# Optimization experiments

Measured on AMD Instinct MI355X. Metric: run time of the kernel, lower is better.

Reference implementation:

```python
import jax, jax.numpy as jnp
import numpy as np

B, T, EPROJS, DUNITS, ATT_DIM, ODIM, LMAX = 16, 800, 512, 1024, 512, 5000, 96
SOS = EOS = ODIM - 1
SCALING = 2.0  # ESPnet AttAdd default softmax scaling


def setup_inputs() -> dict:
    key = jax.random.key(0)
    ks = jax.random.split(key, 16)
    w = lambda i, shape: (jax.random.normal(ks[i], shape, jnp.float32) * 0.02)
    return {
        "hs_pad": jax.random.normal(ks[0], (B, T, EPROJS), jnp.float32),
        "hlens": jnp.full((B,), T, dtype=jnp.int32),
        "ys_pad": jax.random.randint(ks[1], (B, LMAX), 0, ODIM - 2, dtype=jnp.int32),
        "embed": w(2, (ODIM, DUNITS)),
        # layer 0 LSTMCell: input = [embed ; att_context]
        "W_ih0": w(3, (4 * DUNITS, DUNITS + EPROJS)),
        "W_hh0": w(4, (4 * DUNITS, DUNITS)),
        "b_ih0": jnp.zeros((4 * DUNITS,), jnp.float32),
        "b_hh0": jnp.zeros((4 * DUNITS,), jnp.float32),
        # layer 1 LSTMCell
        "W_ih1": w(5, (4 * DUNITS, DUNITS)),
        "W_hh1": w(6, (4 * DUNITS, DUNITS)),
        "b_ih1": jnp.zeros((4 * DUNITS,), jnp.float32),
        "b_hh1": jnp.zeros((4 * DUNITS,), jnp.float32),
        # AttAdd (additive attention)
        "W_enc": w(7, (ATT_DIM, EPROJS)),
        "b_enc": jnp.zeros((ATT_DIM,), jnp.float32),
        "W_dec": w(8, (ATT_DIM, DUNITS)),
        "gvec": w(9, (ATT_DIM,)),
        # output projection (context_residual=False -> dunits -> odim)
        "W_out": w(10, (ODIM, DUNITS)),
        "b_out": jnp.zeros((ODIM,), jnp.float32),
    }


def _lstm_cell(x, h, c, W_ih, W_hh, b_ih, b_hh):
    g = x @ W_ih.T + b_ih + h @ W_hh.T + b_hh  # (B, 4D), torch gate order i,f,g,o
    i, f, gg, o = jnp.split(g, 4, axis=-1)
    c_new = jax.nn.sigmoid(f) * c + jax.nn.sigmoid(i) * jnp.tanh(gg)
    h_new = jax.nn.sigmoid(o) * jnp.tanh(c_new)
    return h_new, c_new


def reference(hs_pad, hlens, ys_pad, embed, W_ih0, W_hh0, b_ih0, b_hh0,
              W_ih1, W_hh1, b_ih1, b_hh1, W_enc, b_enc, W_dec, gvec,
              W_out, b_out):
    batch = ys_pad.shape[0]
    # ys_in = [sos; y], ys_out = [y; eos]  (all targets full length -> no ignore_id)
    sos_col = jnp.full((batch, 1), SOS, dtype=ys_pad.dtype)
    eos_col = jnp.full((batch, 1), EOS, dtype=ys_pad.dtype)
    ys_in = jnp.concatenate([sos_col, ys_pad], axis=1)   # (B, L+1)
    ys_out = jnp.concatenate([ys_pad, eos_col], axis=1)  # (B, L+1)
    olength = ys_out.shape[1]

    eys = embed[ys_in]  # (B, L+1, D)  dropout_emb is identity (p=0)

    # precompute encoder projection for additive attention (done once, as in ESPnet)
    pre_enc = jnp.einsum('bte,ae->bta', hs_pad, W_enc) + b_enc  # (B, T, ATT)
    mask = jnp.arange(hs_pad.shape[1])[None, :] < hlens[:, None]  # (B, T)

    z0 = jnp.zeros((batch, DUNITS), hs_pad.dtype)
    zeros = (z0, z0, z0, z0)  # z0, c0, z1, c1

    def step(carry, ey_t):
        z0, c0, z1, c1 = carry
        # AttAdd: e = gvec . tanh(W_enc h + W_dec z0)
        dec_proj = z0 @ W_dec.T  # (B, ATT)
        e = jnp.tanh(pre_enc + dec_proj[:, None, :]) @ gvec  # (B, T)
        e = jnp.where(mask, e, -jnp.inf)
        att_w = jax.nn.softmax(SCALING * e, axis=-1)
        att_c = jnp.einsum('bt,bte->be', att_w, hs_pad)  # (B, EPROJS)
        x = jnp.concatenate([ey_t, att_c], axis=-1)  # (B, D+EPROJS)
        z0, c0 = _lstm_cell(x, z0, c0, W_ih0, W_hh0, b_ih0, b_hh0)
        z1, c1 = _lstm_cell(z0, z1, c1, W_ih1, W_hh1, b_ih1, b_hh1)
        return (z0, c0, z1, c1), z1

    _, z_all = jax.lax.scan(step, zeros, jnp.swapaxes(eys, 0, 1))  # (L+1, B, D)
    z_all = jnp.swapaxes(z_all, 0, 1)  # (B, L+1, D)

    logits = jnp.einsum('bld,od->blo', z_all, W_out) + b_out  # (B, L+1, ODIM)
    logp = jax.nn.log_softmax(logits, axis=-1)
    nll = -jnp.take_along_axis(logp, ys_out[..., None].astype(jnp.int32), axis=-1)[..., 0]
    loss = jnp.mean(nll)  # reduction='mean' over all tokens (no ignored targets)
    # ESPnet: self.loss *= (mean(len(ys_in)) - 1) = LMAX
    loss = loss * jnp.asarray(LMAX, loss.dtype)
    return loss
```

## Files before the change

kernel.cpp:

```cpp
#include <hip/hip_runtime.h>
#include <stdint.h>

#define Bsz 16
#define Tlen 800
#define EPROJS 512
#define DUNITS 1024
#define ATT 512
#define ODIM 5000
#define LMAX 96
#define OL 97
#define NTOK (OL*Bsz)
#define G4 (4*DUNITS)
#define KX 1536
#define KA1 2048
#define SOS_ID (ODIM-1)
#define NWG 512
#define TCH 25

typedef unsigned short u16;
typedef unsigned int u32;
typedef unsigned long long u64;
typedef short bfrag8 __attribute__((ext_vector_type(8)));
typedef float f32x4 __attribute__((ext_vector_type(4)));

__device__ __forceinline__ float bf2f(u16 u){
  union { uint32_t u; float f; } v; v.u = ((uint32_t)u) << 16; return v.f;
}
__device__ __forceinline__ u16 f2bf(float f){
  union { float f; uint32_t u; } v; v.f = f;
  uint32_t r = v.u + 0x7FFFu + ((v.u >> 16) & 1u);
  return (u16)(r >> 16);
}
__device__ __forceinline__ float sigm(float x){ return 1.0f/(1.0f + __expf(-x)); }
__device__ __forceinline__ float tanh_f(float x){ return 1.0f - 2.0f/(__expf(2.0f*x) + 1.0f); }

__device__ __forceinline__ u64 ald64(const void* p){
  return __hip_atomic_load((const u64*)p, __ATOMIC_RELAXED, __HIP_MEMORY_SCOPE_AGENT);
}
__device__ __forceinline__ void ast64(void* p, u64 v){
  __hip_atomic_store((u64*)p, v, __ATOMIC_RELAXED, __HIP_MEMORY_SCOPE_AGENT);
}
__device__ __forceinline__ float aldf(const float* p){
  return __hip_atomic_load(p, __ATOMIC_RELAXED, __HIP_MEMORY_SCOPE_AGENT);
}
__device__ __forceinline__ void astf(float* p, float v){
  __hip_atomic_store(p, v, __ATOMIC_RELAXED, __HIP_MEMORY_SCOPE_AGENT);
}
__device__ __forceinline__ void ast32(u32* p, u32 v){
  __hip_atomic_store(p, v, __ATOMIC_RELAXED, __HIP_MEMORY_SCOPE_AGENT);
}
__device__ __forceinline__ int ald32(const int* p){
  return __hip_atomic_load(p, __ATOMIC_RELAXED, __HIP_MEMORY_SCOPE_AGENT);
}
__device__ __forceinline__ bfrag8 aldfrag(const u16* p){
  union { u64 q[2]; bfrag8 f; } u;
  u.q[0] = ald64(p);
  u.q[1] = ald64(p + 4);
  return u.f;
}

__device__ __forceinline__ f32x4 mfma_loop_a(const u16* A, int lda,
                                             const u16* Bm, int ldb,
                                             int K, f32x4 acc){
  int lane = threadIdx.x & 63;
  const u16* pa = A + (size_t)(lane & 15) * lda + ((lane >> 4) * 8);
  const u16* pb = Bm + (size_t)(lane & 15) * ldb + ((lane >> 4) * 8);
  #pragma unroll 4
  for (int k = 0; k < K; k += 32){
    bfrag8 av = aldfrag(pa + k);
    bfrag8 bv = *(const bfrag8*)(pb + k);
    acc = __builtin_amdgcn_mfma_f32_16x16x32_bf16(av, bv, acc, 0, 0, 0);
  }
  return acc;
}
__device__ __forceinline__ f32x4 mfma_loop(const u16* A, int lda,
                                           const u16* Bm, int ldb,
                                           int K, f32x4 acc){
  int lane = threadIdx.x & 63;
  const u16* pa = A + (size_t)(lane & 15) * lda + ((lane >> 4) * 8);
  const u16* pb = Bm + (size_t)(lane & 15) * ldb + ((lane >> 4) * 8);
  #pragma unroll 4
  for (int k = 0; k < K; k += 32){
    bfrag8 av = *(const bfrag8*)(pa + k);
    bfrag8 bv = *(const bfrag8*)(pb + k);
    acc = __builtin_amdgcn_mfma_f32_16x16x32_bf16(av, bv, acc, 0, 0, 0);
  }
  return acc;
}

__device__ __forceinline__ void wait_slots(const u64* s64, int n64, int tgt){
  __syncthreads();
  if (threadIdx.x < 64){
    int ln = threadIdx.x;
    bool d0 = (ln >= n64), d1 = (ln + 64 >= n64);
    for(;;){
      if (!d0){ u64 v = ald64(&s64[ln]);
        d0 = ((int)(u32)v >= tgt) && ((int)(u32)(v >> 32) >= tgt); }
      if (!d1){ u64 v = ald64(&s64[ln + 64]);
        d1 = ((int)(u32)v >= tgt) && ((int)(u32)(v >> 32) >= tgt); }
      if (__all(d0 && d1)) break;
      __builtin_amdgcn_s_sleep(1);
    }
  }
  __syncthreads();
}
__device__ __forceinline__ void signal_slot(int* slot, int val){
  __syncthreads();
  if (threadIdx.x == 0) ast32((u32*)slot, (u32)val);
}

__global__ __launch_bounds__(256) void k_zero(float* p, int n){
  int i = blockIdx.x*256 + threadIdx.x;
  if (i < n) p[i] = 0.f;
}
__global__ __launch_bounds__(256) void k_cvt(const float* src, u16* dst, int n){
  int i = blockIdx.x*256 + threadIdx.x, st = gridDim.x*256;
  for (; i < n; i += st) dst[i] = f2bf(src[i]);
}
__global__ __launch_bounds__(256) void k_build_wc0p(const float* Whh0, const float* Wih0, u16* out){
  int i = blockIdx.x*256+threadIdx.x, n = 256*16*KX, st = gridDim.x*256;
  for (; i<n; i+=st){
    int k = i % KX, ws = i / KX;
    int s = ws & 15, w2 = ws >> 4;
    int r = (s>>2)*1024 + 4*w2 + (s&3);
    float v = (k < 1024) ? Whh0[(size_t)r*1024 + k] : Wih0[(size_t)r*KX + k];
    out[i] = f2bf(v);
  }
}
__global__ __launch_bounds__(256) void k_build_wc1p(const float* Wih1, const float* Whh1, u16* out){
  int i = blockIdx.x*256+threadIdx.x, n = 256*16*KA1, st = gridDim.x*256;
  for (; i<n; i+=st){
    int k = i % KA1, ws = i / KA1;
    int s = ws & 15, w2 = ws >> 4;
    int r = (s>>2)*1024 + 4*w2 + (s&3);
    float v = (k < 1024) ? Wih1[(size_t)r*1024 + k] : Whh1[(size_t)r*1024 + (k-1024)];
    out[i] = f2bf(v);
  }
}
__global__ __launch_bounds__(256) void k_build_wih0p(const float* Wih0, u16* out){
  int i = blockIdx.x*256+threadIdx.x, n = 256*16*DUNITS, st = gridDim.x*256;
  for (; i<n; i+=st){
    int k = i % DUNITS, ws = i / DUNITS;
    int s = ws & 15, w2 = ws >> 4;
    int r = (s>>2)*1024 + 4*w2 + (s&3);
    out[i] = f2bf(Wih0[(size_t)r*KX + k]);
  }
}
__global__ __launch_bounds__(256) void k_build_aey(const float* embed, const int* ys_pad, u16* out){
  int i = blockIdx.x*256+threadIdx.x, n = NTOK*DUNITS, st = gridDim.x*256;
  for (; i<n; i+=st){
    int row = i / DUNITS, k = i % DUNITS;
    int l = row / Bsz, b = row % Bsz;
    int idx = (l == 0) ? SOS_ID : ys_pad[b*LMAX + (l-1)];
    out[i] = f2bf(embed[(size_t)idx*DUNITS + k]);
  }
}

__global__ __launch_bounds__(64) void k_gemm_preenc(const u16* hsb, const u16* Wenc,
                                                    const float* b_enc, u16* pre_enc){
  int bid = blockIdx.x;
  int m0 = (bid >> 5) * 16, n0 = (bid & 31) * 16;
  int lane = threadIdx.x & 63;
  int col = n0 + (lane & 15);
  float bias = b_enc[col];
  f32x4 acc = {bias, bias, bias, bias};
  acc = mfma_loop(hsb + (size_t)m0*EPROJS, EPROJS, Wenc + (size_t)n0*EPROJS, EPROJS, EPROJS, acc);
  int quad = lane >> 4;
  #pragma unroll
  for (int r = 0; r < 4; r++)
    pre_enc[(size_t)(m0 + quad*4 + r)*ATT + col] = f2bf(acc[r]);
}

__global__ __launch_bounds__(64) void k_gemm_logits(const u16* zall, const u16* Woutb,
                                                    const float* b_out, float* logits){
  const int NT = 313;
  int bid = blockIdx.x;
  int m0 = (bid / NT) * 16, n0 = (bid % NT) * 16;
  int lane = threadIdx.x & 63;
  int col = n0 + (lane & 15);
  bool ok = col < ODIM;
  int brow = ok ? col : 0;
  float bias = ok ? b_out[col] : 0.f;
  f32x4 acc = {bias, bias, bias, bias};
  const u16* pa = zall + (size_t)m0*DUNITS + (size_t)(lane & 15)*DUNITS + (lane >> 4)*8;
  const u16* pb = Woutb + (size_t)brow*DUNITS + (lane >> 4)*8;
  #pragma unroll 4
  for (int k = 0; k < DUNITS; k += 32){
    bfrag8 av = *(const bfrag8*)(pa + k);
    bfrag8 bv = *(const bfrag8*)(pb + k);
    acc = __builtin_amdgcn_mfma_f32_16x16x32_bf16(av, bv, acc, 0, 0, 0);
  }
  int quad = lane >> 4;
  if (ok){
    #pragma unroll
    for (int r = 0; r < 4; r++)
      logits[(size_t)(m0 + quad*4 + r)*ODIM + col] = acc[r];
  }
}

__global__ __launch_bounds__(256) void k_nll(const float* logits, const int* ys_pad, float* nll){
  int n = blockIdx.x;
  int b = n & 15, l = n >> 4;
  const float* row = logits + (size_t)n * ODIM;
  __shared__ float red[256];
  float m = -1e30f;
  for (int i = threadIdx.x; i < ODIM; i += 256) m = fmaxf(m, row[i]);
  red[threadIdx.x] = m; __syncthreads();
  for (int s = 128; s > 0; s >>= 1){
    if (threadIdx.x < s) red[threadIdx.x] = fmaxf(red[threadIdx.x], red[threadIdx.x + s]);
    __syncthreads();
  }
  float M = red[0]; __syncthreads();
  float sum = 0.f;
  for (int i = threadIdx.x; i < ODIM; i += 256) sum += __expf(row[i] - M);
  red[threadIdx.x] = sum; __syncthreads();
  for (int s = 128; s > 0; s >>= 1){
    if (threadIdx.x < s) red[threadIdx.x] += red[threadIdx.x + s];
    __syncthreads();
  }
  if (threadIdx.x == 0){
    int tgt = (l < LMAX) ? ys_pad[b*LMAX + l] : (ODIM - 1);
    nll[n] = (M + __logf(red[0])) - row[tgt];
  }
}

__global__ __launch_bounds__(256) void k_loss(const float* nll, float* out){
  __shared__ float red[256];
  float s = 0.f;
  for (int i = threadIdx.x; i < NTOK; i += 256) s += nll[i];
  red[threadIdx.x] = s; __syncthreads();
  for (int st = 128; st > 0; st >>= 1){
    if (threadIdx.x < st) red[threadIdx.x] += red[threadIdx.x + st];
    __syncthreads();
  }
  if (threadIdx.x == 0) out[0] = red[0] * ((float)LMAX / (float)NTOK);
}

__global__ __launch_bounds__(256, 2) void k_persist(
  const u16* __restrict__ peb, const u16* __restrict__ hsb,
  const u16* __restrict__ wc0p, const u16* __restrict__ wc1p, const u16* __restrict__ wdecb,
  const u16* __restrict__ wih0p, const u16* __restrict__ aey,
  const float* __restrict__ b_ih0, const float* __restrict__ b_hh0,
  const float* __restrict__ b_ih1, const float* __restrict__ b_hh1,
  const float* __restrict__ gvec, const int* __restrict__ hlens,
  u16* a1b0, u16* a1b1, float* dpbuf, float* part, float* partS, u16* xatt,
  u16* zall, int* bar)
{
  __shared__ __align__(16) u16 s_pe[TCH*512];
  __shared__ __align__(16) u16 s_hs[TCH*512];
  __shared__ __align__(16) float s_dp[512];
  __shared__ __align__(16) float s_gv[512];
  __shared__ __align__(16) float s_red[2048];
  __shared__ float s_c[64];
  __shared__ float s_bias[16];
  __shared__ float s_bias0[16];
  __shared__ float s_sp[4];
  __shared__ __align__(8) u16 s_h[64];

  int tid = threadIdx.x, blk = blockIdx.x;
  int wv = tid >> 6, ln = tid & 63;
  int s2_b = blk >> 5, s2_ch = blk & 31;
  int t0 = s2_ch * TCH;
  int hl = hlens[s2_b];
  bool isLow = (blk < 256);
  int hw = blk - 256;
  bool isdp = (!isLow) && ((hw & 7) == 0);
  int wdp = hw >> 3;

  int* z0s  = bar;
  int* z1s  = bar + 256;
  int* dps  = bar + 512;
  int* atts = bar + 544;
  int* parts= bar + 576;

  {
    const bfrag8* src_pe = (const bfrag8*)(peb + ((size_t)(s2_b*Tlen + t0))*512);
    const bfrag8* src_hs = (const bfrag8*)(hsb + ((size_t)(s2_b*Tlen + t0))*512);
    for (int idx = tid; idx < TCH*512/8; idx += 256){
      ((bfrag8*)s_pe)[idx] = src_pe[idx];
      ((bfrag8*)s_hs)[idx] = src_hs[idx];
    }
    for (int a = tid; a < 512; a += 256) s_gv[a] = gvec[a];
    if (isLow && tid < 16){
      int r = (tid>>2)*1024 + 4*blk + (tid&3);
      s_bias[tid] = b_ih1[r] + b_hh1[r];
    }
    if (!isLow && tid < 16){
      int r = (tid>>2)*1024 + 4*hw + (tid&3);
      s_bias0[tid] = b_ih0[r] + b_hh0[r];
    }
    if (tid < 64) s_c[tid] = 0.f;
  }
  __syncthreads();

  for (int i = 0; i < OL; i++){
    int par = i & 1;
    const u16* a1r = par ? a1b1 : a1b0;
    u16* a1w = par ? a1b0 : a1b1;
    float* dpc   = dpbuf + (size_t)par*(16*512);
    float* partc = part  + (size_t)par*(16*32*512);
    float* pSc   = partS + (size_t)par*(16*32);
    u16*   xac   = xatt  + (size_t)par*(16*512);

    f32x4 acc0 = {0.f,0.f,0.f,0.f};

    if (!isLow){
      if (isdp){
        if (i >= 1){
          const u64* z64 = (const u64*)z0s;
          bool d = (ln >= 32);
          for(;;){
            if (!d){ u64 v = ald64(&z64[wv*32 + ln]);
              d = ((int)(u32)v >= i) && ((int)(u32)(v >> 32) >= i); }
            if (__all(d)) break;
            __builtin_amdgcn_s_sleep(1);
          }
        }
        const u16* btd = wdecb + (size_t)wdp*16*DUNITS;
        f32x4 ad = {0.f,0.f,0.f,0.f};
        ad = mfma_loop_a(a1r + wv*256, KA1, btd + wv*256, DUNITS, 256, ad);
        int q = ln >> 4;
        #pragma unroll
        for (int r = 0; r < 4; r++) s_red[wv*256 + (q*4+r)*16 + (ln & 15)] = ad[r];
        __syncthreads();
        {
          float val = s_red[tid] + s_red[256+tid] + s_red[512+tid] + s_red[768+tid];
          int b = tid >> 4, al = tid & 15;
          astf(&dpc[b*512 + wdp*16 + al], val);
        }
        signal_slot(&dps[wdp], i + 1);
      }
      acc0 = mfma_loop(aey + ((size_t)i*Bsz)*DUNITS + wv*256, DUNITS,
                       wih0p + (size_t)hw*16*DUNITS + wv*256, DUNITS, 256, acc0);
    }

    wait_slots((const u64*)dps, 16, i + 1);
    ((u64*)s_dp)[tid] = ald64(((const u64*)(dpc + s2_b*512)) + tid);
    __syncthreads();
    {
      float dpr[8], gvr[8];
      {
        float4 d1 = *(const float4*)&s_dp[ln*8];
        float4 d2 = *(const float4*)&s_dp[ln*8+4];
        float4 g1 = *(const float4*)&s_gv[ln*8];
        float4 g2 = *(const float4*)&s_gv[ln*8+4];
        dpr[0]=d1.x; dpr[1]=d1.y; dpr[2]=d1.z; dpr[3]=d1.w;
        dpr[4]=d2.x; dpr[5]=d2.y; dpr[6]=d2.z; dpr[7]=d2.w;
        gvr[0]=g1.x; gvr[1]=g1.y; gvr[2]=g1.z; gvr[3]=g1.w;
        gvr[4]=g2.x; gvr[5]=g2.y; gvr[6]=g2.z; gvr[7]=g2.w;
      }
      float attc[8];
      #pragma unroll
      for (int j = 0; j < 8; j++) attc[j] = 0.f;
      float sp = 0.f;
      for (int lt = wv; lt < TCH; lt += 4){
        int t = t0 + lt;
        bool valid = (t < hl);
        float e = 0.f;
        if (valid){
          bfrag8 pv = *(const bfrag8*)&s_pe[lt*512 + ln*8];
          #pragma unroll
          for (int j = 0; j < 8; j++){
            float x = bf2f(((u16*)&pv)[j]) + dpr[j];
            e += gvr[j] * tanh_f(x);
          }
        }
        #pragma unroll
        for (int off = 32; off > 0; off >>= 1) e += __shfl_xor(e, off, 64);
        float p = valid ? __expf(2.0f * e) : 0.f;
        if (ln == 0) sp += p;
        bfrag8 hv = *(const bfrag8*)&s_hs[lt*512 + ln*8];
        #pragma unroll
        for (int j = 0; j < 8; j++) attc[j] += p * bf2f(((u16*)&hv)[j]);
      }
      *(float4*)&s_red[wv*512 + ln*8]     = make_float4(attc[0],attc[1],attc[2],attc[3]);
      *(float4*)&s_red[wv*512 + ln*8 + 4] = make_float4(attc[4],attc[5],attc[6],attc[7]);
      if (ln == 0) s_sp[wv] = sp;
      __syncthreads();
      {
        int e0 = 2*tid;
        float v0 = s_red[e0]   + s_red[512+e0]   + s_red[1024+e0]   + s_red[1536+e0];
        float v1 = s_red[e0+1] + s_red[512+e0+1] + s_red[1024+e0+1] + s_red[1536+e0+1];
        union { float f[2]; u64 q; } pu; pu.f[0]=v0; pu.f[1]=v1;
        ast64(&partc[((size_t)(s2_b*32 + s2_ch))*512 + e0], pu.q);
      }
      if (tid == 0) astf(&pSc[s2_b*32 + s2_ch], s_sp[0]+s_sp[1]+s_sp[2]+s_sp[3]);
      signal_slot(&parts[s2_b*32 + s2_ch], i + 1);
    }

    if (isLow){
      if (blk < 16){
        if (wv == 0){
          const int* myparts = parts + blk*32;
          bool dn = (ln >= 32);
          for(;;){
            if (!dn) dn = (ald32(&myparts[ln]) >= i + 1);
            if (__all(dn)) break;
            __builtin_amdgcn_s_sleep(1);
          }
        }
        __syncthreads();
        float v0 = 0.f, v1 = 0.f;
        const u64* pp = (const u64*)(partc + ((size_t)blk*32)*512) + tid;
        #pragma unroll 8
        for (int c2 = 0; c2 < 32; c2++){
          union { u64 q; float f[2]; } x; x.q = ald64(pp + (size_t)c2*256);
          v0 += x.f[0]; v1 += x.f[1];
        }
        if (wv == 0){
          float sp = (ln < 32) ? aldf(&pSc[blk*32 + ln]) : 0.f;
          #pragma unroll
          for (int off = 32; off > 0; off >>= 1) sp += __shfl_xor(sp, off, 64);
          if (ln == 0) s_sp[0] = 1.0f / sp;
        }
        __syncthreads();
        float rinv = s_sp[0];
        u32 wpk = (u32)f2bf(v0*rinv) | ((u32)f2bf(v1*rinv) << 16);
        ast32(((u32*)xac) + blk*256 + tid, wpk);
        signal_slot(&atts[blk], i + 1);
      }
      if (i >= 1){
        if (i >= 2 && wv >= 2){
          const u64* z64 = (const u64*)z1s;
          bool d = false;
          for(;;){
            if (!d){ u64 v = ald64(&z64[(wv-2)*64 + ln]);
              d = ((int)(u32)v >= i) && ((int)(u32)(v >> 32) >= i); }
            if (__all(d)) break;
            __builtin_amdgcn_s_sleep(1);
          }
        }
        const u16* bt = wc1p + (size_t)blk*16*KA1;
        f32x4 acc = {0.f,0.f,0.f,0.f};
        acc = mfma_loop_a(a1r + wv*512, KA1, bt + wv*512, KA1, 512, acc);
        int q = ln >> 4;
        #pragma unroll
        for (int r = 0; r < 4; r++) s_red[wv*256 + (q*4+r)*16 + (ln & 15)] = acc[r];
        __syncthreads();
        {
          float val = s_red[tid] + s_red[256+tid] + s_red[512+tid] + s_red[768+tid]
                    + s_bias[tid & 15];
          s_red[1024 + tid] = val;
        }
        __syncthreads();
        if (tid < 64){
          int b = tid >> 2, jj = tid & 3;
          float gi = s_red[1024 + b*16 + jj];
          float gf = s_red[1024 + b*16 + 4 + jj];
          float gg = s_red[1024 + b*16 + 8 + jj];
          float go = s_red[1024 + b*16 + 12 + jj];
          float c = s_c[tid];
          float cn = sigm(gf)*c + sigm(gi)*tanh_f(gg);
          float h  = sigm(go)*tanh_f(cn);
          s_c[tid] = cn;
          s_h[tid] = f2bf(h);
        }
        if (wv == 0){
          if (ln < 16){
            u64 hq = ((u64*)s_h)[ln];
            ast64(&a1w[ln*KA1 + 1024 + 4*blk], hq);
            *(u64*)&zall[((size_t)(i-1)*Bsz + ln)*DUNITS + 4*blk] = hq;
          }
          asm volatile("s_waitcnt vmcnt(0)" ::: "memory");
          if (ln == 0) ast32((u32*)&z1s[blk], (u32)(i + 1));
        }
      }
    } else {
      const u16* bt0 = wc0p + (size_t)hw*16*KX;
      acc0 = mfma_loop_a(a1r + wv*256, KA1, bt0 + wv*256, KX, 256, acc0);
      wait_slots((const u64*)atts, 8, i + 1);
      acc0 = mfma_loop_a(xac + wv*128, 512, bt0 + 1024 + wv*128, KX, 128, acc0);
      int q = ln >> 4;
      #pragma unroll
      for (int r = 0; r < 4; r++) s_red[wv*256 + (q*4+r)*16 + (ln & 15)] = acc0[r];
      __syncthreads();
      {
        float val = s_red[tid] + s_red[256+tid] + s_red[512+tid] + s_red[768+tid]
                  + s_bias0[tid & 15];
        s_red[1024 + tid] = val;
      }
      __syncthreads();
      if (tid < 64){
        int b = tid >> 2, jj = tid & 3;
        float gi = s_red[1024 + b*16 + jj];
        float gf = s_red[1024 + b*16 + 4 + jj];
        float gg = s_red[1024 + b*16 + 8 + jj];
        float go = s_red[1024 + b*16 + 12 + jj];
        float c = s_c[tid];
        float cn = sigm(gf)*c + sigm(gi)*tanh_f(gg);
        float h  = sigm(go)*tanh_f(cn);
        s_c[tid] = cn;
        s_h[tid] = f2bf(h);
      }
      if (wv == 0){
        if (ln < 16) ast64(&a1w[ln*KA1 + 4*hw], ((u64*)s_h)[ln]);
        asm volatile("s_waitcnt vmcnt(0)" ::: "memory");
        if (ln == 0) ast32((u32*)&z0s[hw], (u32)(i + 1));
      }
    }
  }

  if (isLow){
    wait_slots((const u64*)z0s, 128, OL);
    wait_slots((const u64*)z1s, 128, OL);
    const u16* a1r = (OL & 1) ? a1b1 : a1b0;
    const u16* bt = wc1p + (size_t)blk*16*KA1;
    f32x4 acc = {0.f,0.f,0.f,0.f};
    acc = mfma_loop_a(a1r + wv*512, KA1, bt + wv*512, KA1, 512, acc);
    int q = ln >> 4;
    #pragma unroll
    for (int r = 0; r < 4; r++) s_red[wv*256 + (q*4+r)*16 + (ln & 15)] = acc[r];
    __syncthreads();
    {
      float val = s_red[tid] + s_red[256+tid] + s_red[512+tid] + s_red[768+tid]
                + s_bias[tid & 15];
      s_red[1024 + tid] = val;
    }
    __syncthreads();
    if (tid < 64){
      int b = tid >> 2, jj = tid & 3;
      float gi = s_red[1024 + b*16 + jj];
      float gf = s_red[1024 + b*16 + 4 + jj];
      float gg = s_red[1024 + b*16 + 8 + jj];
      float go = s_red[1024 + b*16 + 12 + jj];
      float c = s_c[tid];
      float cn = sigm(gf)*c + sigm(gi)*tanh_f(gg);
      float h  = sigm(go)*tanh_f(cn);
      s_h[tid] = f2bf(h);
    }
    __syncthreads();
    if (tid < 16)
      *(u64*)&zall[((size_t)LMAX*Bsz + tid)*DUNITS + 4*blk] = ((u64*)s_h)[tid];
  }
}

extern "C" void kernel_launch(void* const* d_in, const int* in_sizes, int n_in,
                              void* d_out, int out_size, void* d_ws, size_t ws_size,
                              hipStream_t stream)
{
  const float* hs     = (const float*)d_in[0];
  const int*   hlens  = (const int*)d_in[1];
  const int*   ys_pad = (const int*)d_in[2];
  const float* embed  = (const float*)d_in[3];
  const float* W_ih0  = (const float*)d_in[4];
  const float* W_hh0  = (const float*)d_in[5];
  const float* b_ih0  = (const float*)d_in[6];
  const float* b_hh0  = (const float*)d_in[7];
  const float* W_ih1  = (const float*)d_in[8];
  const float* W_hh1  = (const float*)d_in[9];
  const float* b_ih1  = (const float*)d_in[10];
  const float* b_hh1  = (const float*)d_in[11];
  const float* W_enc  = (const float*)d_in[12];
  const float* b_enc  = (const float*)d_in[13];
  const float* W_dec  = (const float*)d_in[14];
  const float* gvec   = (const float*)d_in[15];
  const float* W_out  = (const float*)d_in[16];
  const float* b_out  = (const float*)d_in[17];
  (void)in_sizes; (void)n_in; (void)out_size; (void)ws_size;

  char* w = (char*)d_ws;
  size_t off = 0;
  auto alloc = [&](size_t bytes)->char*{
    char* ptr = w + off;
    off += (bytes + 255) & ~(size_t)255;
    return ptr;
  };
  int*   bar  = (int*)alloc(8192);
  u16*  a1b0  = (u16*)alloc(Bsz*KA1*2);
  u16*  a1b1  = (u16*)alloc(Bsz*KA1*2);
  size_t state_bytes = off;
  float* dpbuf = (float*)alloc(2*(size_t)Bsz*ATT*4);
  float* part  = (float*)alloc(2*(size_t)Bsz*32*512*4);
  float* partS = (float*)alloc(2*(size_t)Bsz*32*4);
  u16*  xatt   = (u16*)alloc(2*(size_t)Bsz*512*2);
  u16*  hsb    = (u16*)alloc((size_t)Bsz*Tlen*EPROJS*2);
  u16*  peb    = (u16*)alloc((size_t)Bsz*Tlen*ATT*2);
  u16*  wencb  = (u16*)alloc((size_t)ATT*EPROJS*2);
  u16*  wdecb  = (u16*)alloc((size_t)ATT*DUNITS*2);
  u16*  wc0p   = (u16*)alloc((size_t)G4*KX*2);
  u16*  wc1p   = (u16*)alloc((size_t)G4*KA1*2);
  u16*  wih0p  = (u16*)alloc((size_t)G4*DUNITS*2);
  u16*  woutb  = (u16*)alloc((size_t)ODIM*DUNITS*2);
  u16*  aey    = (u16*)alloc((size_t)NTOK*DUNITS*2);
  u16*  zall   = (u16*)alloc((size_t)NTOK*DUNITS*2);
  float* logits= (float*)alloc((size_t)NTOK*ODIM*4);
  float* nll   = (float*)alloc(NTOK*4);

  {
    int n = (int)(state_bytes / 4);
    k_zero<<<(n + 255)/256, 256, 0, stream>>>((float*)w, n);
  }

  k_cvt<<<2048,256,0,stream>>>(hs, hsb, Bsz*Tlen*EPROJS);
  k_cvt<<<256,256,0,stream>>>(W_enc, wencb, ATT*EPROJS);
  k_cvt<<<512,256,0,stream>>>(W_dec, wdecb, ATT*DUNITS);
  k_cvt<<<2048,256,0,stream>>>(W_out, woutb, ODIM*DUNITS);
  k_build_wc0p<<<4096,256,0,stream>>>(W_hh0, W_ih0, wc0p);
  k_build_wc1p<<<4096,256,0,stream>>>(W_ih1, W_hh1, wc1p);
  k_build_wih0p<<<4096,256,0,stream>>>(W_ih0, wih0p);
  k_build_aey<<<1024,256,0,stream>>>(embed, ys_pad, aey);

  k_gemm_preenc<<<(Bsz*Tlen/16)*(ATT/16), 64, 0, stream>>>(hsb, wencb, b_enc, peb);

  {
    void* args[] = {
      (void*)&peb, (void*)&hsb, (void*)&wc0p, (void*)&wc1p, (void*)&wdecb,
      (void*)&wih0p, (void*)&aey, (void*)&b_ih0, (void*)&b_hh0,
      (void*)&b_ih1, (void*)&b_hh1, (void*)&gvec, (void*)&hlens,
      (void*)&a1b0, (void*)&a1b1, (void*)&dpbuf, (void*)&part, (void*)&partS,
      (void*)&xatt, (void*)&zall, (void*)&bar
    };
    hipLaunchCooperativeKernel((const void*)k_persist, dim3(NWG), dim3(256),
                               args, 0, stream);
  }

  k_gemm_logits<<<OL*313, 64, 0, stream>>>(zall, woutb, b_out, logits);
  k_nll<<<NTOK,256,0,stream>>>(logits, ys_pad, nll);
  k_loss<<<1,256,0,stream>>>(nll, (float*)d_out);
}
```

Measured before the change: 3.288 ms.

## Replace flag-based signaling with step-tagged 64-bit data words in persistent kernel

The dec-proj and attention-context exchange buffers now pack each value with its step index into one 64-bit word. Consumers poll the data words directly instead of waiting on separate slot flags and then reading the data, which removes a round trip and the flag stores. The partial-sum reduction also issues all 32 loads before accumulating, and the MFMA loops are unrolled further. The tagged buffers double the bytes moved and rely on 64-bit atomic stores being observed as a single unit. They also increase register pressure in the polling loops.

```diff
diff --git a/kernel.cpp b/kernel.cpp
--- a/kernel.cpp
+++ b/kernel.cpp
@@ -65,7 +65,7 @@
   int lane = threadIdx.x & 63;
   const u16* pa = A + (size_t)(lane & 15) * lda + ((lane >> 4) * 8);
   const u16* pb = Bm + (size_t)(lane & 15) * ldb + ((lane >> 4) * 8);
-  #pragma unroll 4
+  #pragma unroll 8
   for (int k = 0; k < K; k += 32){
     bfrag8 av = aldfrag(pa + k);
     bfrag8 bv = *(const bfrag8*)(pb + k);
@@ -79,7 +79,7 @@
   int lane = threadIdx.x & 63;
   const u16* pa = A + (size_t)(lane & 15) * lda + ((lane >> 4) * 8);
   const u16* pb = Bm + (size_t)(lane & 15) * ldb + ((lane >> 4) * 8);
-  #pragma unroll 4
+  #pragma unroll 8
   for (int k = 0; k < K; k += 32){
     bfrag8 av = *(const bfrag8*)(pa + k);
     bfrag8 bv = *(const bfrag8*)(pb + k);
@@ -243,7 +243,7 @@
   const float* __restrict__ b_ih0, const float* __restrict__ b_hh0,
   const float* __restrict__ b_ih1, const float* __restrict__ b_hh1,
   const float* __restrict__ gvec, const int* __restrict__ hlens,
-  u16* a1b0, u16* a1b1, float* dpbuf, float* part, float* partS, u16* xatt,
+  u16* a1b0, u16* a1b1, u64* dpt, float* part, float* partS, u64* xat,
   u16* zall, int* bar)
 {
   __shared__ __align__(16) u16 s_pe[TCH*512];
@@ -269,8 +269,6 @@
 
   int* z0s  = bar;
   int* z1s  = bar + 256;
-  int* dps  = bar + 512;
-  int* atts = bar + 544;
   int* parts= bar + 576;
 
   {
@@ -297,10 +295,11 @@
     int par = i & 1;
     const u16* a1r = par ? a1b1 : a1b0;
     u16* a1w = par ? a1b0 : a1b1;
-    float* dpc   = dpbuf + (size_t)par*(16*512);
+    u64*  dptc  = dpt + (size_t)par*(16*512);
     float* partc = part  + (size_t)par*(16*32*512);
     float* pSc   = partS + (size_t)par*(16*32);
-    u16*   xac   = xatt  + (size_t)par*(16*512);
+    u64*  xatc  = xat + (size_t)par*(16*256);
+    u32 tgt = (u32)(i + 1);
 
     f32x4 acc0 = {0.f,0.f,0.f,0.f};
 
@@ -326,16 +325,26 @@
         {
           float val = s_red[tid] + s_red[256+tid] + s_red[512+tid] + s_red[768+tid];
           int b = tid >> 4, al = tid & 15;
-          astf(&dpc[b*512 + wdp*16 + al], val);
-        }
-        signal_slot(&dps[wdp], i + 1);
+          union { float f; u32 u; } uv; uv.f = val;
+          ast64(&dptc[b*512 + wdp*16 + al], ((u64)tgt << 32) | uv.u);
+        }
       }
       acc0 = mfma_loop(aey + ((size_t)i*Bsz)*DUNITS + wv*256, DUNITS,
                        wih0p + (size_t)hw*16*DUNITS + wv*256, DUNITS, 256, acc0);
     }
 
-    wait_slots((const u64*)dps, 16, i + 1);
-    ((u64*)s_dp)[tid] = ald64(((const u64*)(dpc + s2_b*512)) + tid);
+    {
+      const u64* db = dptc + (size_t)s2_b*512;
+      u64 w0 = 0, w1 = 0; bool d0 = false, d1 = false;
+      for(;;){
+        if (!d0){ u64 v = ald64(&db[2*tid]);   if ((u32)(v>>32) >= tgt){ w0=v; d0=true; } }
+        if (!d1){ u64 v = ald64(&db[2*tid+1]); if ((u32)(v>>32) >= tgt){ w1=v; d1=true; } }
+        if (__all(d0 && d1)) break;
+        __builtin_amdgcn_s_sleep(2);
+      }
+      union { u32 u; float f; } c0, c1; c0.u = (u32)w0; c1.u = (u32)w1;
+      s_dp[2*tid] = c0.f; s_dp[2*tid+1] = c1.f;
+    }
     __syncthreads();
     {
       float dpr[8], gvr[8];
@@ -401,11 +410,16 @@
         }
         __syncthreads();
         float v0 = 0.f, v1 = 0.f;
-        const u64* pp = (const u64*)(partc + ((size_t)blk*32)*512) + tid;
-        #pragma unroll 8
-        for (int c2 = 0; c2 < 32; c2++){
-          union { u64 q; float f[2]; } x; x.q = ald64(pp + (size_t)c2*256);
-          v0 += x.f[0]; v1 += x.f[1];
+        {
+          const u64* pp = (const u64*)(partc + ((size_t)blk*32)*512) + tid;
+          u64 wq[32];
+          #pragma unroll
+          for (int c2 = 0; c2 < 32; c2++) wq[c2] = ald64(pp + (size_t)c2*256);
+          #pragma unroll
+          for (int c2 = 0; c2 < 32; c2++){
+            union { u64 q; float f[2]; } x; x.q = wq[c2];
+            v0 += x.f[0]; v1 += x.f[1];
+          }
         }
         if (wv == 0){
           float sp = (ln < 32) ? aldf(&pSc[blk*32 + ln]) : 0.f;
@@ -415,9 +429,8 @@
         }
         __syncthreads();
         float rinv = s_sp[0];
-        u32 wpk = (u32)f2bf(v0*rinv) | ((u32)f2bf(v1*rinv) << 16);
-        ast32(((u32*)xac) + blk*256 + tid, wpk);
-        signal_slot(&atts[blk], i + 1);
+        u32 pk = (u32)f2bf(v0*rinv) | ((u32)f2bf(v1*rinv) << 16);
+        ast64(&xatc[(size_t)blk*256 + tid], ((u64)tgt << 32) | pk);
       }
       if (i >= 1){
         if (i >= 2 && wv >= 2){
@@ -468,8 +481,36 @@
     } else {
       const u16* bt0 = wc0p + (size_t)hw*16*KX;
       acc0 = mfma_loop_a(a1r + wv*256, KA1, bt0 + wv*256, KX, 256, acc0);
-      wait_slots((const u64*)atts, 8, i + 1);
-      acc0 = mfma_loop_a(xac + wv*128, 512, bt0 + 1024 + wv*128, KX, 128, acc0);
+      u64 xw[16];
+      {
+        const u64* xp = xatc + (size_t)(ln & 15)*256 + wv*64 + ((ln >> 4)*4);
+        bool dny[16];
+        #pragma unroll
+        for (int m = 0; m < 16; m++) dny[m] = false;
+        for(;;){
+          bool allr = true;
+          #pragma unroll
+          for (int m = 0; m < 16; m++){
+            if (!dny[m]){
+              u64 v = ald64(&xp[(m >> 2)*16 + (m & 3)]);
+              if ((u32)(v>>32) >= tgt){ xw[m] = v; dny[m] = true; } else allr = false;
+            }
+          }
+          if (__all(allr)) break;
+          __builtin_amdgcn_s_sleep(2);
+        }
+      }
+      {
+        const u16* pb = bt0 + 1024 + wv*128 + (size_t)(ln & 15)*KX + ((ln >> 4)*8);
+        #pragma unroll
+        for (int ks = 0; ks < 4; ks++){
+          union { u32 q[4]; bfrag8 f; } fa;
+          #pragma unroll
+          for (int j = 0; j < 4; j++) fa.q[j] = (u32)xw[ks*4 + j];
+          bfrag8 bv = *(const bfrag8*)(pb + ks*32);
+          acc0 = __builtin_amdgcn_mfma_f32_16x16x32_bf16(fa.f, bv, acc0, 0, 0, 0);
+        }
+      }
       int q = ln >> 4;
       #pragma unroll
       for (int r = 0; r < 4; r++) s_red[wv*256 + (q*4+r)*16 + (ln & 15)] = acc0[r];
@@ -568,11 +609,11 @@
   int*   bar  = (int*)alloc(8192);
   u16*  a1b0  = (u16*)alloc(Bsz*KA1*2);
   u16*  a1b1  = (u16*)alloc(Bsz*KA1*2);
+  u64*  dpt   = (u64*)alloc(2*(size_t)Bsz*ATT*8);
+  u64*  xat   = (u64*)alloc(2*(size_t)Bsz*256*8);
   size_t state_bytes = off;
-  float* dpbuf = (float*)alloc(2*(size_t)Bsz*ATT*4);
   float* part  = (float*)alloc(2*(size_t)Bsz*32*512*4);
   float* partS = (float*)alloc(2*(size_t)Bsz*32*4);
-  u16*  xatt   = (u16*)alloc(2*(size_t)Bsz*512*2);
   u16*  hsb    = (u16*)alloc((size_t)Bsz*Tlen*EPROJS*2);
   u16*  peb    = (u16*)alloc((size_t)Bsz*Tlen*ATT*2);
   u16*  wencb  = (u16*)alloc((size_t)ATT*EPROJS*2);
@@ -607,8 +648,8 @@
       (void*)&peb, (void*)&hsb, (void*)&wc0p, (void*)&wc1p, (void*)&wdecb,
       (void*)&wih0p, (void*)&aey, (void*)&b_ih0, (void*)&b_hh0,
       (void*)&b_ih1, (void*)&b_hh1, (void*)&gvec, (void*)&hlens,
-      (void*)&a1b0, (void*)&a1b1, (void*)&dpbuf, (void*)&part, (void*)&partS,
-      (void*)&xatt, (void*)&zall, (void*)&bar
+      (void*)&a1b0, (void*)&a1b1, (void*)&dpt, (void*)&part, (void*)&partS,
+      (void*)&xat, (void*)&zall, (void*)&bar
     };
     hipLaunchCooperativeKernel((const void*)k_persist, dim3(NWG), dim3(256),
                                args, 0, stream);
```

Measured after the change: 3.373 ms. +2.6%, slower.
